# Performance work log

Measured on AMD Instinct MI355X. Metric: run time of the kernel, lower is better.

## Reference

```python
import jax, jax.numpy as jnp
import numpy as np

B, TIN, N, F = 2, 12, 800, 2
H, D = 6, 8
C = H * D          # 48
TP = 10            # prediction steps (= pre_step)
PS5 = TP // 5      # int(pre_step/5) = 2
KW = PS5 + 12      # conv1 kernel width = 14


def setup_inputs() -> dict:
    key = jax.random.key(0)
    it = iter(jax.random.split(key, 40))
    def rn(shape, s=0.1):
        return jax.random.normal(next(it), shape, dtype=jnp.float32) * s
    inp = {}
    inp['x'] = rn((B, TIN, N, F), 1.0)
    inp['T'] = rn((B, TP, N, F - 1), 1.0)
    inp['adj'] = jnp.ones((N, N), dtype=bool)  # softmax(laplace) != 0 is all-True
    for nm in ['Wq_t', 'Wk_t', 'Wv_t', 'Wq_st', 'Wk_st', 'Wv_st']:
        inp[nm] = rn((H, F, D))
    for nm in ['bq_t', 'bk_t', 'bv_t', 'bq_st', 'bk_st', 'bv_st']:
        inp[nm] = rn((H, D))
    inp['conv1_w'] = rn((C, F, 1, KW))
    inp['conv1_b'] = rn((C,))
    inp['Wproj_t'] = rn((C, C)); inp['bproj_t'] = rn((C,))
    inp['Wproj_st'] = rn((C, C)); inp['bproj_st'] = rn((C,))
    for nm in ['xhr_wz', 'xhr_wr', 'xhr_wh']:
        inp[nm] = rn((TIN, 3 * C, C))     # input 2C concat hidden C
    for nm in ['xhr_bz', 'xhr_br', 'xhr_bh']:
        inp[nm] = rn((TIN, N, C))
    for nm in ['last_wz', 'last_wr', 'last_wh']:
        inp[nm] = rn((TP, 2 * C, C))      # input C concat hidden C
    for nm in ['last_bz', 'last_br', 'last_bh']:
        inp[nm] = rn((TP, N, C))
    inp['Wout'] = rn((C, 1)); inp['bout'] = rn((1,))
    return inp


def _gru(xi, h, wz, bz, wr, br, wh, bh):
    xh = jnp.concatenate([xi, h], axis=-1)
    z = jax.nn.sigmoid(xh @ wz + bz)
    r = jax.nn.sigmoid(xh @ wr + br)
    hh = jnp.tanh(jnp.concatenate([xi, r * h], axis=-1) @ wh + bh)
    return (1.0 - z) * h + z * hh


def _forward(adj, x, T, Wq_t, bq_t, Wk_t, bk_t, Wv_t, bv_t,
             Wq_st, bq_st, Wk_st, bk_st, Wv_st, bv_st,
             conv1_w, conv1_b, Wproj_t, bproj_t, Wproj_st, bproj_st,
             xhr_wz, xhr_bz, xhr_wr, xhr_br, xhr_wh, xhr_bh,
             last_wz, last_bz, last_wr, last_br, last_wh, last_bh, Wout, bout):
    scale = 1.0 / np.sqrt(D)
    adjf = adj.astype(jnp.float32)
    # ---- temporal multi-head attention (causal over time, per node) ----
    q = jnp.einsum('btnf,hfd->btnhd', x, Wq_t) + bq_t
    k = jnp.einsum('btnf,hfd->btnhd', x, Wk_t) + bk_t
    v = jnp.einsum('btnf,hfd->btnhd', x, Wv_t) + bv_t
    s = jnp.einsum('btnhd,bsnhd->bnhts', q, k) * scale
    causal = jnp.tril(jnp.ones((TIN, TIN), dtype=bool))
    s = jnp.where(causal, s, -1e9)
    p = jax.nn.softmax(s, axis=-1)
    att_t = jnp.einsum('bnhts,bsnhd->btnhd', p, v).reshape(B, TIN, N, C)
    # ---- spatial multi-head attention (adjacency-weighted, per timestep) ----
    q = jnp.einsum('btnf,hfd->btnhd', x, Wq_st) + bq_st
    k = jnp.einsum('btnf,hfd->btnhd', x, Wk_st) + bk_st
    v = jnp.einsum('btnf,hfd->btnhd', x, Wv_st) + bv_st
    s = jnp.einsum('btnhd,btmhd->bthnm', q, k) * scale
    s = s * adjf  # multiplicative adjacency mask (NOT -inf fill), as in source
    p = jax.nn.softmax(s, axis=-1)
    att_st = jnp.einsum('bthnm,btmhd->btnhd', p, v).reshape(B, TIN, N, C)
    att_stt = jnp.concatenate([att_t @ Wproj_t + bproj_t,
                               att_st @ Wproj_st + bproj_st], axis=-1)  # [B,TIN,N,2C]
    # ---- encoder GRU stack over timesteps 1..TIN-1, cell i has own weights ----
    h0 = jnp.zeros((B, N, C), dtype=x.dtype)
    seq = jnp.swapaxes(att_stt[:, 1:], 0, 1)  # [TIN-1, B, N, 2C]
    def step(h, inp):
        xi, wz, bz, wr, br, wh, bh = inp
        return _gru(xi, h, wz, bz, wr, br, wh, bh), None
    ht, _ = jax.lax.scan(step, h0, (seq, xhr_wz[1:], xhr_bz[1:], xhr_wr[1:],
                                    xhr_br[1:], xhr_wh[1:], xhr_bh[1:]))
    # ---- conv1 over time-extended input ----
    Tcat = jnp.concatenate([jnp.zeros(T.shape[:-1] + (1,), T.dtype), T], axis=-1)
    tpx = jnp.concatenate([x, Tcat], axis=1)                 # [B, TIN+TP, N, F]
    tpx = jnp.concatenate([tpx, tpx[:, :PS5 - 1]], axis=1)   # [B, TIN+TP+PS5-1, N, F]
    lhs = jnp.transpose(tpx, (0, 3, 2, 1))                   # [B, F, N, Ttot]
    conv = jax.lax.conv_general_dilated(lhs, conv1_w, (1, 1), 'VALID',
                                        dimension_numbers=('NCHW', 'OIHW', 'NCHW'))
    pre = jnp.transpose(conv + conv1_b[None, :, None, None], (0, 3, 2, 1))  # [B,TP,N,C]
    # ---- decoder GRU, one cell per step, collecting states ----
    def step2(h, inp):
        xi, wz, bz, wr, br, wh, bh = inp
        h = _gru(xi, h, wz, bz, wr, br, wh, bh)
        return h, h
    _, outs = jax.lax.scan(step2, ht, (jnp.swapaxes(pre, 0, 1), last_wz, last_bz,
                                       last_wr, last_br, last_wh, last_bh))
    out = jnp.swapaxes(outs, 0, 1)  # [B, TP, N, C]
    return out @ Wout + bout        # [B, TP, N, 1]


def reference(x, T, adj, Wq_t, bq_t, Wk_t, bk_t, Wv_t, bv_t,
              Wq_st, bq_st, Wk_st, bk_st, Wv_st, bv_st,
              conv1_w, conv1_b, Wproj_t, bproj_t, Wproj_st, bproj_st,
              xhr_wz, xhr_bz, xhr_wr, xhr_br, xhr_wh, xhr_bh,
              last_wz, last_bz, last_wr, last_br, last_wh, last_bh, Wout, bout):
    return _forward(adj, x, T, Wq_t, bq_t, Wk_t, bk_t, Wv_t, bv_t,
                    Wq_st, bq_st, Wk_st, bk_st, Wv_st, bv_st,
                    conv1_w, conv1_b, Wproj_t, bproj_t, Wproj_st, bproj_st,
                    xhr_wz, xhr_bz, xhr_wr, xhr_br, xhr_wh, xhr_bh,
                    last_wz, last_bz, last_wr, last_br, last_wh, last_bh, Wout, bout)
```

## Files before the change

kernel.cpp:

```cpp
#include <hip/hip_runtime.h>
#include <hip/hip_bf16.h>

typedef __hip_bfloat16 bf16;
typedef __attribute__((ext_vector_type(8))) short s8b;
typedef __attribute__((ext_vector_type(4))) float f4;

#define B_ 2
#define TIN_ 12
#define N_ 800
#define F_ 2
#define H_ 6
#define D_ 8
#define C_ 48
#define TP_ 10
#define KW_ 14
#define SCALE 0.35355339059327373f
#define LOG2E 1.4426950408889634f

__device__ __forceinline__ float sigm(float x) { return 1.0f / (1.0f + __expf(-x)); }
__device__ __forceinline__ float tanh_(float x) {
  float e = __expf(-2.0f * x);
  return 2.0f / (1.0f + e) - 1.0f;
}
__device__ __forceinline__ float exp2_(float x) { return __builtin_amdgcn_exp2f(x); }
__device__ __forceinline__ float bfu(unsigned short u) {
  return __uint_as_float((unsigned)u << 16);
}
__device__ __forceinline__ unsigned short f2u(float v) {
  return __bfloat16_as_ushort(__float2bfloat16(v));
}
__device__ __forceinline__ float ldc(const float* p, size_t i) { return p[i]; }
__device__ __forceinline__ float ldc(const bf16* p, size_t i) { return __bfloat162float(p[i]); }
__device__ __forceinline__ void sto(float* p, size_t i, float v) { p[i] = v; }
__device__ __forceinline__ void sto(bf16* p, size_t i, float v) { p[i] = __float2bfloat16(v); }
__device__ __forceinline__ void gll16(const void* g, void* l) {
  __builtin_amdgcn_global_load_lds(
      (__attribute__((address_space(1))) void*)(g),
      (__attribute__((address_space(3))) void*)(l), 16, 0, 0);
}
__device__ __forceinline__ int detect_f32(const void* xv) {
  const unsigned int* xw = (const unsigned int*)xv;
  unsigned int w = xw[threadIdx.x & 63];
  int e = (w >> 7) & 0xFF;
  int bad = ((e >= 1 && e < 96) || (e > 150)) ? 1 : 0;
  unsigned long long m = __ballot(bad);
  return (__popcll(m) >= 16) ? 1 : 0;
}

template <typename TI>
__device__ __forceinline__ void pack_body(
    int gid, const TI* xwz, const TI* xwr, const TI* xwh,
    const TI* lwz, const TI* lwr, const TI* lwh, bf16* pwb) {
  const int total = 21 * 9216;
  if (gid >= total) return;
  int step = gid / 9216, r = gid % 9216;
  int g = r / 3072;  r %= 3072;
  int nt = r / 1024; r %= 1024;
  int c = r / 512;   r %= 512;
  int lane = r / 8, j = r % 8;
  int k = 32 * c + (lane >> 4) * 8 + j;
  int n = nt * 16 + (lane & 15);
  float v = 0.f;
  if (k < 48) {
    if (step < 11) {
      int t = step + 1;
      const TI* w = (g == 0) ? xwz : (g == 1) ? xwr : xwh;
      v = ldc(w, ((size_t)t * 144 + 96 + k) * 48 + n);
    } else {
      int t = step - 11;
      const TI* w = (g == 0) ? lwz : (g == 1) ? lwr : lwh;
      v = ldc(w, ((size_t)t * 96 + 48 + k) * 48 + n);
    }
  }
  pwb[gid] = __float2bfloat16(v);
}

template <typename TI>
__device__ __forceinline__ void temporal_body(
    int gid, const TI* x, const TI* Wq, const TI* Wk, const TI* Wv,
    const TI* bq, const TI* bk, const TI* bv, bf16* att_t) {
  const int total = B_ * (TIN_ - 1) * H_ * N_;
  if (gid >= total) return;
  int n = gid % N_;
  int r = gid / N_;
  int h = r % H_;  r /= H_;
  int t = (r % (TIN_ - 1)) + 1;
  int b = r / (TIN_ - 1);

  float wq[F_][D_], wk[F_][D_], wv[F_][D_], bqv[D_], bkv[D_], bvv[D_];
#pragma unroll
  for (int f = 0; f < F_; ++f)
#pragma unroll
    for (int d = 0; d < D_; ++d) {
      wq[f][d] = ldc(Wq, (h * F_ + f) * D_ + d);
      wk[f][d] = ldc(Wk, (h * F_ + f) * D_ + d);
      wv[f][d] = ldc(Wv, (h * F_ + f) * D_ + d);
    }
#pragma unroll
  for (int d = 0; d < D_; ++d) {
    bqv[d] = ldc(bq, h * D_ + d);
    bkv[d] = ldc(bk, h * D_ + d);
    bvv[d] = ldc(bv, h * D_ + d);
  }
  float xt0 = ldc(x, ((b * TIN_ + t) * N_ + n) * F_ + 0);
  float xt1 = ldc(x, ((b * TIN_ + t) * N_ + n) * F_ + 1);
  float q[D_];
#pragma unroll
  for (int d = 0; d < D_; ++d) q[d] = xt0 * wq[0][d] + xt1 * wq[1][d] + bqv[d];

  float sc[TIN_];
  float mx = -1e30f;
#pragma unroll
  for (int s = 0; s < TIN_; ++s) {
    float xs0 = ldc(x, ((b * TIN_ + s) * N_ + n) * F_ + 0);
    float xs1 = ldc(x, ((b * TIN_ + s) * N_ + n) * F_ + 1);
    float dot = 0.f;
#pragma unroll
    for (int d = 0; d < D_; ++d)
      dot += q[d] * (xs0 * wk[0][d] + xs1 * wk[1][d] + bkv[d]);
    dot *= SCALE;
    sc[s] = (s <= t) ? dot : -1e30f;
    mx = fmaxf(mx, sc[s]);
  }
  float sum = 0.f;
#pragma unroll
  for (int s = 0; s < TIN_; ++s) {
    float p = __expf(sc[s] - mx);
    sc[s] = p;
    sum += p;
  }
  float inv = 1.0f / sum;
  float acc[D_];
#pragma unroll
  for (int d = 0; d < D_; ++d) acc[d] = 0.f;
#pragma unroll
  for (int s = 0; s < TIN_; ++s) {
    float xs0 = ldc(x, ((b * TIN_ + s) * N_ + n) * F_ + 0);
    float xs1 = ldc(x, ((b * TIN_ + s) * N_ + n) * F_ + 1);
#pragma unroll
    for (int d = 0; d < D_; ++d)
      acc[d] += sc[s] * (xs0 * wv[0][d] + xs1 * wv[1][d] + bvv[d]);
  }
  bf16* o = att_t + ((size_t)((b * 11 + (t - 1)) * N_ + n)) * C_ + h * D_;
#pragma unroll
  for (int d = 0; d < D_; ++d) o[d] = __float2bfloat16(acc[d] * inv);
}

template <typename TI>
__device__ __forceinline__ void spatial4_body(
    float2* xs, float (*M)[9], float (*Vw)[3][D_],
    int tile, int ty, int b, int hg,
    const TI* x, const TI* Wq, const TI* Wk, const TI* Wv,
    const TI* bq, const TI* bk, const TI* bv, bf16* att_st) {
  int t = ty + 1;
  int tid = threadIdx.x;

  for (int m = tid; m < N_; m += 832)
    xs[m] = make_float2(ldc(x, ((b * TIN_ + t) * N_ + m) * F_ + 0),
                        ldc(x, ((b * TIN_ + t) * N_ + m) * F_ + 1));
  if (tid < 18) {
    int lh = tid / 9, e = tid % 9, a = e / 3, bb = e % 3;
    int h = hg * 2 + lh;
    float acc = 0.f;
    for (int d = 0; d < 8; ++d) {
      float qa = (a == 0) ? ldc(Wq, (h * 2 + 0) * 8 + d)
               : (a == 1) ? ldc(Wq, (h * 2 + 1) * 8 + d) : ldc(bq, h * 8 + d);
      float kb = (bb == 0) ? ldc(Wk, (h * 2 + 0) * 8 + d)
               : (bb == 1) ? ldc(Wk, (h * 2 + 1) * 8 + d) : ldc(bk, h * 8 + d);
      acc += qa * kb;
    }
    M[lh][e] = acc * SCALE * LOG2E;
  }
  if (tid >= 64 && tid < 64 + 48) {
    int e = tid - 64;
    int lh = e / 24, a = (e % 24) / 8, d = e % 8;
    int h = hg * 2 + lh;
    Vw[lh][a][d] = (a == 0) ? ldc(Wv, (h * 2 + 0) * 8 + d)
                 : (a == 1) ? ldc(Wv, (h * 2 + 1) * 8 + d) : ldc(bv, h * 8 + d);
  }
  __syncthreads();
  if (tid < 800) {
    int row = tid >> 3, ms = tid & 7;
    int n = tile * 100 + row;
    float x0 = xs[n].x, x1 = xs[n].y;
    float A[2], Bc[2], Cc[2];
#pragma unroll
    for (int lh = 0; lh < 2; ++lh) {
      A[lh]  = M[lh][0] * x0 + M[lh][3] * x1 + M[lh][6];
      Bc[lh] = M[lh][1] * x0 + M[lh][4] * x1 + M[lh][7];
      Cc[lh] = M[lh][2] * x0 + M[lh][5] * x1 + M[lh][8];
    }
    float Sp[2] = {0, 0}, S0[2] = {0, 0}, S1[2] = {0, 0};
    for (int m = ms * 100; m < ms * 100 + 100; ++m) {
      float2 xm = xs[m];
#pragma unroll
      for (int lh = 0; lh < 2; ++lh) {
        float p = exp2_(A[lh] * xm.x + Bc[lh] * xm.y + Cc[lh]);
        Sp[lh] += p;
        S0[lh] += p * xm.x;
        S1[lh] += p * xm.y;
      }
    }
#pragma unroll
    for (int lh = 0; lh < 2; ++lh) {
#pragma unroll
      for (int off = 1; off < 8; off <<= 1) {
        Sp[lh] += __shfl_xor(Sp[lh], off);
        S0[lh] += __shfl_xor(S0[lh], off);
        S1[lh] += __shfl_xor(S1[lh], off);
      }
    }
    if (ms == 0) {
      bf16* o = att_st + ((size_t)((b * 11 + ty) * N_ + n)) * C_;
#pragma unroll
      for (int lh = 0; lh < 2; ++lh) {
        int h = hg * 2 + lh;
        float inv = 1.f / Sp[lh];
#pragma unroll
        for (int d = 0; d < 8; ++d)
          o[h * 8 + d] = __float2bfloat16(
              (S0[lh] * Vw[lh][0][d] + S1[lh] * Vw[lh][1][d] + Sp[lh] * Vw[lh][2][d]) * inv);
      }
    }
  }
}

#define SP_BLKS 528
#define TMP_BLKS 127
#define PK_BLKS 233
__global__ __launch_bounds__(832) void k_phase1(
    const void* x,
    const void* Wq_t, const void* Wk_t, const void* Wv_t,
    const void* bq_t, const void* bk_t, const void* bv_t,
    const void* Wq_st, const void* Wk_st, const void* Wv_st,
    const void* bq_st, const void* bk_st, const void* bv_st,
    const void* xwz, const void* xwr, const void* xwh,
    const void* lwz, const void* lwr, const void* lwh,
    bf16* att_t, bf16* att_st, bf16* pwb) {
  __shared__ float2 xs[N_];
  __shared__ float M[2][9];
  __shared__ float Vw[2][3][D_];
  int f32 = detect_f32(x);
  int bx = blockIdx.x;
  if (bx < SP_BLKS) {
    int tile = bx % 8, ty = (bx / 8) % 11, zz = bx / 88;
    int b = zz / 3, hg = zz % 3;
    if (f32)
      spatial4_body<float>(xs, M, Vw, tile, ty, b, hg,
                           (const float*)x, (const float*)Wq_st, (const float*)Wk_st,
                           (const float*)Wv_st, (const float*)bq_st, (const float*)bk_st,
                           (const float*)bv_st, att_st);
    else
      spatial4_body<bf16>(xs, M, Vw, tile, ty, b, hg,
                          (const bf16*)x, (const bf16*)Wq_st, (const bf16*)Wk_st,
                          (const bf16*)Wv_st, (const bf16*)bq_st, (const bf16*)bk_st,
                          (const bf16*)bv_st, att_st);
  } else if (bx < SP_BLKS + TMP_BLKS) {
    int gid = (bx - SP_BLKS) * 832 + threadIdx.x;
    if (f32)
      temporal_body<float>(gid, (const float*)x, (const float*)Wq_t, (const float*)Wk_t,
                           (const float*)Wv_t, (const float*)bq_t, (const float*)bk_t,
                           (const float*)bv_t, att_t);
    else
      temporal_body<bf16>(gid, (const bf16*)x, (const bf16*)Wq_t, (const bf16*)Wk_t,
                          (const bf16*)Wv_t, (const bf16*)bq_t, (const bf16*)bk_t,
                          (const bf16*)bv_t, att_t);
  } else {
    int gid = (bx - SP_BLKS - TMP_BLKS) * 832 + threadIdx.x;
    if (f32)
      pack_body<float>(gid, (const float*)xwz, (const float*)xwr, (const float*)xwh,
                       (const float*)lwz, (const float*)lwr, (const float*)lwh, pwb);
    else
      pack_body<bf16>(gid, (const bf16*)xwz, (const bf16*)xwr, (const bf16*)xwh,
                      (const bf16*)lwz, (const bf16*)lwr, (const bf16*)lwh, pwb);
  }
}

template <typename TI>
__device__ __forceinline__ void projx2_body(
    unsigned short (*rawT)[72], unsigned short (*rawS)[72], unsigned short (*catS)[104],
    int tile, int ty, int b,
    const bf16* att_t, const bf16* att_st,
    const TI* Wpt, const TI* bpt, const TI* Wps, const TI* bps,
    const TI* xwz, const TI* xwr, const TI* xwh,
    const TI* xbz, const TI* xbr, const TI* xbh,
    bf16* xfrag) {
  int t = ty + 1;
  int tid = threadIdx.x;
  int wv = tid >> 6, l = tid & 63;
  int cg = l >> 4, cl = l & 15;

  for (int e = tid; e < 64 * 72; e += 192) {
    int rr = e / 72, c = e % 72;
    int n = tile * 64 + rr; if (n > 799) n = 799;
    size_t base = ((size_t)((b * 11 + ty) * N_ + n)) * C_;
    rawT[rr][c] = (c < 48) ? __bfloat16_as_ushort(att_t[base + c]) : (unsigned short)0;
    rawS[rr][c] = (c < 48) ? __bfloat16_as_ushort(att_st[base + c]) : (unsigned short)0;
  }
  __syncthreads();
#pragma unroll
  for (int q = 0; q < 2; ++q) {
    int nt = 2 * wv + q;
    int half = nt / 3;
    int ncol = (nt - half * 3) * 16 + cl;
    float bias = half ? ldc(bps, ncol) : ldc(bpt, ncol);
    s8b Bf0, Bf1;
#pragma unroll
    for (int j = 0; j < 8; ++j) {
      int k0 = cg * 8 + j;
      int k1 = 32 + cg * 8 + j;
      Bf0[j] = (short)f2u(half ? ldc(Wps, (size_t)k0 * 48 + ncol)
                               : ldc(Wpt, (size_t)k0 * 48 + ncol));
      Bf1[j] = (k1 < 48) ? (short)f2u(half ? ldc(Wps, (size_t)k1 * 48 + ncol)
                                           : ldc(Wpt, (size_t)k1 * 48 + ncol))
                         : (short)0;
    }
    unsigned short (*raw)[72] = half ? rawS : rawT;
#pragma unroll
    for (int mt = 0; mt < 4; ++mt) {
      s8b A0 = *(const s8b*)&raw[mt * 16 + cl][cg * 8];
      s8b A1 = *(const s8b*)&raw[mt * 16 + cl][32 + cg * 8];
      f4 acc = {bias, bias, bias, bias};
      acc = __builtin_amdgcn_mfma_f32_16x16x32_bf16(A0, Bf0, acc, 0, 0, 0);
      acc = __builtin_amdgcn_mfma_f32_16x16x32_bf16(A1, Bf1, acc, 0, 0, 0);
#pragma unroll
      for (int r = 0; r < 4; ++r)
        catS[mt * 16 + cg * 4 + r][nt * 16 + cl] = f2u(acc[r]);
    }
  }
  __syncthreads();
#pragma unroll
  for (int q = 0; q < 3; ++q) {
    int nt = 3 * wv + q;
    int g = nt / 3;
    int jj = (nt - g * 3) * 16 + cl;
    const TI* wx = (g == 0) ? xwz : (g == 1) ? xwr : xwh;
    const TI* bx = (g == 0) ? xbz : (g == 1) ? xbr : xbh;
    s8b Bf[3];
#pragma unroll
    for (int c = 0; c < 3; ++c)
#pragma unroll
      for (int j = 0; j < 8; ++j) {
        int k = c * 32 + cg * 8 + j;
        Bf[c][j] = (short)f2u(ldc(wx, ((size_t)t * 144 + k) * 48 + jj));
      }
#pragma unroll
    for (int mt = 0; mt < 4; ++mt) {
      int nbase = tile * 64 + mt * 16;
      if (nbase >= 800) continue;
      s8b A0 = *(const s8b*)&catS[mt * 16 + cl][cg * 8];
      s8b A1 = *(const s8b*)&catS[mt * 16 + cl][32 + cg * 8];
      s8b A2 = *(const s8b*)&catS[mt * 16 + cl][64 + cg * 8];
      f4 acc;
#pragma unroll
      for (int r = 0; r < 4; ++r)
        acc[r] = ldc(bx, ((size_t)t * N_ + (nbase + cg * 4 + r)) * C_ + jj);
      acc = __builtin_amdgcn_mfma_f32_16x16x32_bf16(A0, Bf[0], acc, 0, 0, 0);
      acc = __builtin_amdgcn_mfma_f32_16x16x32_bf16(A1, Bf[1], acc, 0, 0, 0);
      acc = __builtin_amdgcn_mfma_f32_16x16x32_bf16(A2, Bf[2], acc, 0, 0, 0);
      int grp = b * 50 + tile * 4 + mt;
      size_t idx = ((((size_t)grp * 21 + ty) * 9 + nt) * 64 + l) * 4;
      ushort4 u;
      u.x = f2u(acc[0]); u.y = f2u(acc[1]); u.z = f2u(acc[2]); u.w = f2u(acc[3]);
      *(ushort4*)((unsigned short*)xfrag + idx) = u;
    }
  }
}

template <typename TI>
__device__ __forceinline__ void convx5_body(
    float (*tpw)[KW_][2], float (*cw)[KW_][48], unsigned short (*preS)[72],
    int tile, int t, int b,
    const TI* x, const TI* T,
    const TI* conv1_w, const TI* conv1_b,
    const TI* lwz, const TI* lwr, const TI* lwh,
    const TI* lbz, const TI* lbr, const TI* lbh,
    bf16* xfrag) {
  int tid = threadIdx.x;
  int wv = tid >> 6, l = tid & 63;
  int cg = l >> 4, cl = l & 15;
  int rw = tid / 12, jl = tid % 12;

#pragma unroll 7
  for (int p = 0; p < 7; ++p) {
    int e = tid + p * 192;
    int f = e / (KW_ * 48), rem = e % (KW_ * 48), k = rem / 48, c = rem % 48;
    cw[f][k][c] = ldc(conv1_w, (c * F_ + f) * KW_ + k);
  }
#pragma unroll 10
  for (int p = 0; p < 10; ++p) {
    int e = tid + p * 192;
    if (e < 64 * KW_ * 2) {
      int rr = e / (KW_ * 2), rem = e % (KW_ * 2), k = rem / 2, f = rem % 2;
      int n = tile * 64 + rr; if (n > 799) n = 799;
      int tau = t + k;
      float v;
      if (tau < TIN_) v = ldc(x, ((size_t)(b * TIN_ + tau) * N_ + n) * F_ + f);
      else if (tau < TIN_ + TP_) v = (f == 0) ? 0.f : ldc(T, (size_t)(b * TP_ + (tau - TIN_)) * N_ + n);
      else v = ldc(x, ((size_t)(b * TIN_ + 0) * N_ + n) * F_ + f);
      tpw[rr][k][f] = v;
    }
  }
  for (int e = tid; e < 64 * 24; e += 192)
    preS[e / 24][48 + e % 24] = 0;
  __syncthreads();
  {
    int c0 = jl * 4;
    float acc[4][4];
#pragma unroll
    for (int qq = 0; qq < 4; ++qq)
#pragma unroll
      for (int m = 0; m < 4; ++m) acc[qq][m] = ldc(conv1_b, c0 + m);
#pragma unroll
    for (int f = 0; f < 2; ++f)
      for (int k = 0; k < KW_; ++k) {
        const float4 w4 = *(const float4*)&cw[f][k][c0];
        float wvv[4] = {w4.x, w4.y, w4.z, w4.w};
#pragma unroll
        for (int qq = 0; qq < 4; ++qq) {
          float tv = tpw[rw * 4 + qq][k][f];
#pragma unroll
          for (int m = 0; m < 4; ++m) acc[qq][m] += tv * wvv[m];
        }
      }
#pragma unroll
    for (int qq = 0; qq < 4; ++qq)
#pragma unroll
      for (int m = 0; m < 4; ++m)
        preS[rw * 4 + qq][c0 + m] = f2u(acc[qq][m]);
  }
  __syncthreads();
#pragma unroll
  for (int q = 0; q < 3; ++q) {
    int nt = 3 * wv + q;
    int g = nt / 3;
    int jj = (nt - g * 3) * 16 + cl;
    const TI* wl = (g == 0) ? lwz : (g == 1) ? lwr : lwh;
    const TI* bl = (g == 0) ? lbz : (g == 1) ? lbr : lbh;
    s8b Bf0, Bf1;
#pragma unroll
    for (int j = 0; j < 8; ++j) {
      int k0 = cg * 8 + j;
      int k1 = 32 + cg * 8 + j;
      Bf0[j] = (short)f2u(ldc(wl, ((size_t)t * 96 + k0) * 48 + jj));
      Bf1[j] = (k1 < 48) ? (short)f2u(ldc(wl, ((size_t)t * 96 + k1) * 48 + jj)) : (short)0;
    }
#pragma unroll
    for (int mt = 0; mt < 4; ++mt) {
      int nbase = tile * 64 + mt * 16;
      if (nbase >= 800) continue;
      s8b A0 = *(const s8b*)&preS[mt * 16 + cl][cg * 8];
      s8b A1 = *(const s8b*)&preS[mt * 16 + cl][32 + cg * 8];
      f4 acc;
#pragma unroll
      for (int r = 0; r < 4; ++r)
        acc[r] = ldc(bl, ((size_t)t * N_ + (nbase + cg * 4 + r)) * C_ + jj);
      acc = __builtin_amdgcn_mfma_f32_16x16x32_bf16(A0, Bf0, acc, 0, 0, 0);
      acc = __builtin_amdgcn_mfma_f32_16x16x32_bf16(A1, Bf1, acc, 0, 0, 0);
      int grp = b * 50 + tile * 4 + mt;
      size_t idx = ((((size_t)grp * 21 + (11 + t)) * 9 + nt) * 64 + l) * 4;
      ushort4 u;
      u.x = f2u(acc[0]); u.y = f2u(acc[1]); u.z = f2u(acc[2]); u.w = f2u(acc[3]);
      *(ushort4*)((unsigned short*)xfrag + idx) = u;
    }
  }
}

#define PJ_BLKS 286
#define CV_BLKS 260
__global__ __launch_bounds__(192) void k_xc(
    const bf16* att_t, const bf16* att_st,
    const void* Wpt, const void* bpt, const void* Wps, const void* bps,
    const void* xwz, const void* xwr, const void* xwh,
    const void* xbz, const void* xbr, const void* xbh,
    const void* x, const void* T, const void* cw_, const void* cb,
    const void* lwz, const void* lwr, const void* lwh,
    const void* lbz, const void* lbr, const void* lbh, bf16* xfrag) {
  __shared__ __align__(16) char smem[31744];
  int f32 = detect_f32(x);
  int bx = blockIdx.x;
  if (bx < PJ_BLKS) {
    int tile = bx % 13, ty = (bx / 13) % 11, b = bx / 143;
    auto rawT = (unsigned short(*)[72])smem;
    auto rawS = (unsigned short(*)[72])(smem + 9216);
    auto catS = (unsigned short(*)[104])(smem + 18432);
    if (f32)
      projx2_body<float>(rawT, rawS, catS, tile, ty, b, att_t, att_st,
                         (const float*)Wpt, (const float*)bpt, (const float*)Wps,
                         (const float*)bps, (const float*)xwz, (const float*)xwr,
                         (const float*)xwh, (const float*)xbz, (const float*)xbr,
                         (const float*)xbh, xfrag);
    else
      projx2_body<bf16>(rawT, rawS, catS, tile, ty, b, att_t, att_st,
                        (const bf16*)Wpt, (const bf16*)bpt, (const bf16*)Wps,
                        (const bf16*)bps, (const bf16*)xwz, (const bf16*)xwr,
                        (const bf16*)xwh, (const bf16*)xbz, (const bf16*)xbr,
                        (const bf16*)xbh, xfrag);
  } else {
    int cblk = bx - PJ_BLKS;
    int tile = cblk % 13, t = (cblk / 13) % 10, b = cblk / 130;
    auto tpw  = (float(*)[KW_][2])smem;
    auto cw   = (float(*)[KW_][48])(smem + 7168);
    auto preS = (unsigned short(*)[72])(smem + 12544);
    if (f32)
      convx5_body<float>(tpw, cw, preS, tile, t, b,
                         (const float*)x, (const float*)T, (const float*)cw_, (const float*)cb,
                         (const float*)lwz, (const float*)lwr, (const float*)lwh,
                         (const float*)lbz, (const float*)lbr, (const float*)lbh, xfrag);
    else
      convx5_body<bf16>(tpw, cw, preS, tile, t, b,
                        (const bf16*)x, (const bf16*)T, (const bf16*)cw_, (const bf16*)cb,
                        (const bf16*)lwz, (const bf16*)lwr, (const bf16*)lwh,
                        (const bf16*)lbz, (const bf16*)lbr, (const bf16*)lbh, xfrag);
  }
}

template <typename TI, typename TO>
__device__ __forceinline__ void gru11_body(
    unsigned short (*wbuf)[9216], unsigned short (*xbuf)[2560],
    unsigned short* hT, unsigned short* rhT,
    const unsigned short* xfrag, const unsigned short* pwb,
    const TI* Wout, const TI* bout, TO* out) {
  int l = threadIdx.x;
  int cg = l >> 4, cl = l & 15;
  int blk = blockIdx.x;
  int b = blk / 50;
  int n0 = (blk % 50) * 16;

  for (int e = l; e < 1152; e += 64) { hT[e] = 0; rhT[e] = 0; }
  float bo = ldc(bout, 0);
  s8b WoB0, WoB1;
#pragma unroll
  for (int j = 0; j < 8; ++j) {
    int k0 = cg * 8 + j;
    int k1 = 32 + cg * 8 + j;
    WoB0[j] = (cl == 0) ? (short)f2u(ldc(Wout, k0)) : (short)0;
    WoB1[j] = (cl == 0 && k1 < 48) ? (short)f2u(ldc(Wout, k1)) : (short)0;
  }
  float ho[3][4];
#pragma unroll
  for (int nt = 0; nt < 3; ++nt)
#pragma unroll
    for (int r = 0; r < 4; ++r) ho[nt][r] = 0.f;

  const unsigned short* xg = xfrag + (size_t)blk * 48384;
#pragma unroll
  for (int i = 0; i < 18; ++i) gll16(pwb + i * 512 + l * 8, &wbuf[0][i * 512]);
#pragma unroll
  for (int i = 0; i < 5; ++i) gll16(xg + i * 512 + l * 8, &xbuf[0][i * 512]);
  asm volatile("" ::: "memory");

  for (int step = 0; step < 21; ++step) {
    int cur = step & 1;
    s8b hA0 = *(const s8b*)&hT[cl * 72 + cg * 8];
    s8b hA1 = *(const s8b*)&hT[cl * 72 + 32 + cg * 8];
    if (step >= 12) {
      f4 oacc = {bo, bo, bo, bo};
      oacc = __builtin_amdgcn_mfma_f32_16x16x32_bf16(hA0, WoB0, oacc, 0, 0, 0);
      oacc = __builtin_amdgcn_mfma_f32_16x16x32_bf16(hA1, WoB1, oacc, 0, 0, 0);
      if (cl == 0) {
        int t = step - 12;
#pragma unroll
        for (int r = 0; r < 4; ++r)
          sto(out, ((size_t)b * TP_ + t) * N_ + n0 + cg * 4 + r, oacc[r]);
      }
    }
    asm volatile("s_waitcnt vmcnt(0)" ::: "memory");
    s8b Wz[3][2], Wr[3][2], Wh[3][2];
    const unsigned short* wb = wbuf[cur];
#pragma unroll
    for (int nt = 0; nt < 3; ++nt)
#pragma unroll
      for (int c = 0; c < 2; ++c) {
        Wz[nt][c] = *(const s8b*)&wb[0 * 3072 + nt * 1024 + c * 512 + l * 8];
        Wr[nt][c] = *(const s8b*)&wb[1 * 3072 + nt * 1024 + c * 512 + l * 8];
        Wh[nt][c] = *(const s8b*)&wb[2 * 3072 + nt * 1024 + c * 512 + l * 8];
      }
    ushort4 cx[9];
#pragma unroll
    for (int gn = 0; gn < 9; ++gn)
      cx[gn] = *(const ushort4*)&xbuf[cur][gn * 256 + l * 4];
    if (step < 20) {
      const unsigned short* wsn = pwb + (size_t)(step + 1) * 9216;
#pragma unroll
      for (int i = 0; i < 18; ++i) gll16(wsn + i * 512 + l * 8, &wbuf[cur ^ 1][i * 512]);
      const unsigned short* xsn = xg + (size_t)(step + 1) * 2304;
#pragma unroll
      for (int i = 0; i < 5; ++i) gll16(xsn + i * 512 + l * 8, &xbuf[cur ^ 1][i * 512]);
    }
    f4 az[3], ar[3];
#pragma unroll
    for (int nt = 0; nt < 3; ++nt) {
      f4 cz = {bfu(cx[nt].x), bfu(cx[nt].y), bfu(cx[nt].z), bfu(cx[nt].w)};
      cz = __builtin_amdgcn_mfma_f32_16x16x32_bf16(hA0, Wz[nt][0], cz, 0, 0, 0);
      cz = __builtin_amdgcn_mfma_f32_16x16x32_bf16(hA1, Wz[nt][1], cz, 0, 0, 0);
      az[nt] = cz;
      f4 cr = {bfu(cx[3 + nt].x), bfu(cx[3 + nt].y), bfu(cx[3 + nt].z), bfu(cx[3 + nt].w)};
      cr = __builtin_amdgcn_mfma_f32_16x16x32_bf16(hA0, Wr[nt][0], cr, 0, 0, 0);
      cr = __builtin_amdgcn_mfma_f32_16x16x32_bf16(hA1, Wr[nt][1], cr, 0, 0, 0);
      ar[nt] = cr;
    }
    float z[3][4];
#pragma unroll
    for (int nt = 0; nt < 3; ++nt)
#pragma unroll
      for (int r = 0; r < 4; ++r) {
        z[nt][r] = sigm(az[nt][r]);
        float rv = sigm(ar[nt][r]) * ho[nt][r];
        rhT[(cg * 4 + r) * 72 + nt * 16 + cl] = f2u(rv);
      }
    asm volatile("" ::: "memory");
    s8b rA0 = *(const s8b*)&rhT[cl * 72 + cg * 8];
    s8b rA1 = *(const s8b*)&rhT[cl * 72 + 32 + cg * 8];
    f4 ah[3];
#pragma unroll
    for (int nt = 0; nt < 3; ++nt) {
      f4 ch = {bfu(cx[6 + nt].x), bfu(cx[6 + nt].y), bfu(cx[6 + nt].z), bfu(cx[6 + nt].w)};
      ch = __builtin_amdgcn_mfma_f32_16x16x32_bf16(rA0, Wh[nt][0], ch, 0, 0, 0);
      ch = __builtin_amdgcn_mfma_f32_16x16x32_bf16(rA1, Wh[nt][1], ch, 0, 0, 0);
      ah[nt] = ch;
    }
#pragma unroll
    for (int nt = 0; nt < 3; ++nt)
#pragma unroll
      for (int r = 0; r < 4; ++r) {
        float hn = (1.f - z[nt][r]) * ho[nt][r] + z[nt][r] * tanh_(ah[nt][r]);
        ho[nt][r] = hn;
        hT[(cg * 4 + r) * 72 + nt * 16 + cl] = f2u(hn);
      }
    asm volatile("" ::: "memory");
  }
  {
    s8b hA0 = *(const s8b*)&hT[cl * 72 + cg * 8];
    s8b hA1 = *(const s8b*)&hT[cl * 72 + 32 + cg * 8];
    f4 oacc = {bo, bo, bo, bo};
    oacc = __builtin_amdgcn_mfma_f32_16x16x32_bf16(hA0, WoB0, oacc, 0, 0, 0);
    oacc = __builtin_amdgcn_mfma_f32_16x16x32_bf16(hA1, WoB1, oacc, 0, 0, 0);
    if (cl == 0) {
#pragma unroll
      for (int r = 0; r < 4; ++r)
        sto(out, ((size_t)b * TP_ + 9) * N_ + n0 + cg * 4 + r, oacc[r]);
    }
  }
}
__global__ __launch_bounds__(64) void k_gru11(
    const void* xin, const bf16* xfrag, const bf16* pwb,
    const void* Wout, const void* bout, void* out) {
  __shared__ alignas(16) unsigned short wbuf[2][9216];
  __shared__ alignas(16) unsigned short xbuf[2][2560];
  __shared__ alignas(16) unsigned short hT[1152];
  __shared__ alignas(16) unsigned short rhT[1152];
  int f32 = detect_f32(xin);
  if (f32)
    gru11_body<float, float>(wbuf, xbuf, hT, rhT,
                             (const unsigned short*)xfrag, (const unsigned short*)pwb,
                             (const float*)Wout, (const float*)bout, (float*)out);
  else
    gru11_body<bf16, bf16>(wbuf, xbuf, hT, rhT,
                           (const unsigned short*)xfrag, (const unsigned short*)pwb,
                           (const bf16*)Wout, (const bf16*)bout, (bf16*)out);
}

extern "C" void kernel_launch(void* const* d_in, const int* in_sizes, int n_in,
                              void* d_out, int out_size, void* d_ws, size_t ws_size,
                              hipStream_t stream) {
  (void)in_sizes; (void)n_in; (void)out_size; (void)ws_size;
  const void* x       = d_in[0];
  const void* T       = d_in[1];
  const void* Wq_t    = d_in[3];
  const void* Wk_t    = d_in[4];
  const void* Wv_t    = d_in[5];
  const void* Wq_st   = d_in[6];
  const void* Wk_st   = d_in[7];
  const void* Wv_st   = d_in[8];
  const void* bq_t    = d_in[9];
  const void* bk_t    = d_in[10];
  const void* bv_t    = d_in[11];
  const void* bq_st   = d_in[12];
  const void* bk_st   = d_in[13];
  const void* bv_st   = d_in[14];
  const void* conv1_w = d_in[15];
  const void* conv1_b = d_in[16];
  const void* Wproj_t = d_in[17];
  const void* bproj_t = d_in[18];
  const void* Wproj_st= d_in[19];
  const void* bproj_st= d_in[20];
  const void* xhr_wz  = d_in[21];
  const void* xhr_wr  = d_in[22];
  const void* xhr_wh  = d_in[23];
  const void* xhr_bz  = d_in[24];
  const void* xhr_br  = d_in[25];
  const void* xhr_bh  = d_in[26];
  const void* last_wz = d_in[27];
  const void* last_wr = d_in[28];
  const void* last_wh = d_in[29];
  const void* last_bz = d_in[30];
  const void* last_br = d_in[31];
  const void* last_bh = d_in[32];
  const void* Wout    = d_in[33];
  const void* bout    = d_in[34];

  char* wsb = (char*)d_ws;
  bf16* att_t  = (bf16*)(wsb + 256);
  bf16* att_st = att_t + (size_t)2 * 11 * 800 * 48;
  bf16* xfrag  = att_st + (size_t)2 * 11 * 800 * 48;
  bf16* pwb    = xfrag + (size_t)100 * 21 * 9 * 64 * 4;

  k_phase1<<<SP_BLKS + TMP_BLKS + PK_BLKS, 832, 0, stream>>>(
      x, Wq_t, Wk_t, Wv_t, bq_t, bk_t, bv_t,
      Wq_st, Wk_st, Wv_st, bq_st, bk_st, bv_st,
      xhr_wz, xhr_wr, xhr_wh, last_wz, last_wr, last_wh,
      att_t, att_st, pwb);
  k_xc<<<PJ_BLKS + CV_BLKS, 192, 0, stream>>>(
      att_t, att_st, Wproj_t, bproj_t, Wproj_st, bproj_st,
      xhr_wz, xhr_wr, xhr_wh, xhr_bz, xhr_br, xhr_bh,
      x, T, conv1_w, conv1_b, last_wz, last_wr, last_wh,
      last_bz, last_br, last_bh, xfrag);
  k_gru11<<<100, 64, 0, stream>>>(
      x, xfrag, pwb, Wout, bout, d_out);
}
```

Before: 119.9 us.

## Prefetch GRU weights and inputs into registers instead of LDS double buffer

The recurrent GRU kernel no longer uses global_load_lds double buffering with explicit vmcnt waits. It loads the next step's weight fragments and input fragments straight into a second register set, then swaps the A/B sets across an unrolled pair of steps. Empty asm pins keep the loads from being sunk, so their latency hides behind the current step's MFMA and activation work. This removes the LDS round trip and the full memory wait at the top of each step, at the cost of many more VGPRs.

```diff
diff --git a/kernel.cpp b/kernel.cpp
--- a/kernel.cpp
+++ b/kernel.cpp
@@ -17,6 +17,8 @@
 #define SCALE 0.35355339059327373f
 #define LOG2E 1.4426950408889634f
 
+#define PIN(v) asm volatile("" :: "v"(v))
+
 __device__ __forceinline__ float sigm(float x) { return 1.0f / (1.0f + __expf(-x)); }
 __device__ __forceinline__ float tanh_(float x) {
   float e = __expf(-2.0f * x);
@@ -33,11 +35,6 @@
 __device__ __forceinline__ float ldc(const bf16* p, size_t i) { return __bfloat162float(p[i]); }
 __device__ __forceinline__ void sto(float* p, size_t i, float v) { p[i] = v; }
 __device__ __forceinline__ void sto(bf16* p, size_t i, float v) { p[i] = __float2bfloat16(v); }
-__device__ __forceinline__ void gll16(const void* g, void* l) {
-  __builtin_amdgcn_global_load_lds(
-      (__attribute__((address_space(1))) void*)(g),
-      (__attribute__((address_space(3))) void*)(l), 16, 0, 0);
-}
 __device__ __forceinline__ int detect_f32(const void* xv) {
   const unsigned int* xw = (const unsigned int*)xv;
   unsigned int w = xw[threadIdx.x & 63];
@@ -515,9 +512,97 @@
   }
 }
 
+template <bool PF, typename TO>
+__device__ __forceinline__ void gru_step12(
+    int step, int l, int cg, int cl, int b, int n0,
+    s8b (&Wzc)[3][2], s8b (&Wrc)[3][2], s8b (&Whc)[3][2], ushort4 (&cxc)[9],
+    s8b (&Wzn)[3][2], s8b (&Wrn)[3][2], s8b (&Whn)[3][2], ushort4 (&cxn)[9],
+    const unsigned short* pwb, const unsigned short* xg,
+    unsigned short* hT, unsigned short* rhT,
+    float (&ho)[3][4], const s8b& WoB0, const s8b& WoB1, float bo, TO* out) {
+  s8b hA0 = *(const s8b*)&hT[cl * 72 + cg * 8];
+  s8b hA1 = *(const s8b*)&hT[cl * 72 + 32 + cg * 8];
+  if (step >= 12) {
+    f4 oacc = {bo, bo, bo, bo};
+    oacc = __builtin_amdgcn_mfma_f32_16x16x32_bf16(hA0, WoB0, oacc, 0, 0, 0);
+    oacc = __builtin_amdgcn_mfma_f32_16x16x32_bf16(hA1, WoB1, oacc, 0, 0, 0);
+    if (cl == 0) {
+      int t = step - 12;
+#pragma unroll
+      for (int r = 0; r < 4; ++r)
+        sto(out, ((size_t)b * TP_ + t) * N_ + n0 + cg * 4 + r, oacc[r]);
+    }
+  }
+  if (PF) {
+    const unsigned short* pb = pwb + (size_t)(step + 1) * 9216 + (size_t)l * 8;
+#pragma unroll
+    for (int nt = 0; nt < 3; ++nt)
+#pragma unroll
+      for (int c = 0; c < 2; ++c) {
+        Wzn[nt][c] = *(const s8b*)(pb + 0 * 3072 + nt * 1024 + c * 512);
+        Wrn[nt][c] = *(const s8b*)(pb + 1 * 3072 + nt * 1024 + c * 512);
+        Whn[nt][c] = *(const s8b*)(pb + 2 * 3072 + nt * 1024 + c * 512);
+      }
+    const unsigned short* xsrc = xg + (size_t)(step + 1) * 2304 + (size_t)l * 4;
+#pragma unroll
+    for (int gn = 0; gn < 9; ++gn)
+      cxn[gn] = *(const ushort4*)(xsrc + gn * 256);
+  }
+  f4 az[3], ar[3];
+#pragma unroll
+  for (int nt = 0; nt < 3; ++nt) {
+    f4 cz = {bfu(cxc[nt].x), bfu(cxc[nt].y), bfu(cxc[nt].z), bfu(cxc[nt].w)};
+    cz = __builtin_amdgcn_mfma_f32_16x16x32_bf16(hA0, Wzc[nt][0], cz, 0, 0, 0);
+    cz = __builtin_amdgcn_mfma_f32_16x16x32_bf16(hA1, Wzc[nt][1], cz, 0, 0, 0);
+    az[nt] = cz;
+    f4 cr = {bfu(cxc[3 + nt].x), bfu(cxc[3 + nt].y), bfu(cxc[3 + nt].z), bfu(cxc[3 + nt].w)};
+    cr = __builtin_amdgcn_mfma_f32_16x16x32_bf16(hA0, Wrc[nt][0], cr, 0, 0, 0);
+    cr = __builtin_amdgcn_mfma_f32_16x16x32_bf16(hA1, Wrc[nt][1], cr, 0, 0, 0);
+    ar[nt] = cr;
+  }
+  float z[3][4];
+#pragma unroll
+  for (int nt = 0; nt < 3; ++nt)
+#pragma unroll
+    for (int r = 0; r < 4; ++r) {
+      z[nt][r] = sigm(az[nt][r]);
+      float rv = sigm(ar[nt][r]) * ho[nt][r];
+      rhT[(cg * 4 + r) * 72 + nt * 16 + cl] = f2u(rv);
+    }
+  asm volatile("" ::: "memory");
+  s8b rA0 = *(const s8b*)&rhT[cl * 72 + cg * 8];
+  s8b rA1 = *(const s8b*)&rhT[cl * 72 + 32 + cg * 8];
+  f4 ah[3];
+#pragma unroll
+  for (int nt = 0; nt < 3; ++nt) {
+    f4 ch = {bfu(cxc[6 + nt].x), bfu(cxc[6 + nt].y), bfu(cxc[6 + nt].z), bfu(cxc[6 + nt].w)};
+    ch = __builtin_amdgcn_mfma_f32_16x16x32_bf16(rA0, Whc[nt][0], ch, 0, 0, 0);
+    ch = __builtin_amdgcn_mfma_f32_16x16x32_bf16(rA1, Whc[nt][1], ch, 0, 0, 0);
+    ah[nt] = ch;
+  }
+#pragma unroll
+  for (int nt = 0; nt < 3; ++nt)
+#pragma unroll
+    for (int r = 0; r < 4; ++r) {
+      float hn = (1.f - z[nt][r]) * ho[nt][r] + z[nt][r] * tanh_(ah[nt][r]);
+      ho[nt][r] = hn;
+      hT[(cg * 4 + r) * 72 + nt * 16 + cl] = f2u(hn);
+    }
+  asm volatile("" ::: "memory");
+  if (PF) {
+#pragma unroll
+    for (int nt = 0; nt < 3; ++nt)
+#pragma unroll
+      for (int c = 0; c < 2; ++c) {
+        PIN(Wzn[nt][c]); PIN(Wrn[nt][c]); PIN(Whn[nt][c]);
+      }
+#pragma unroll
+    for (int gn = 0; gn < 9; ++gn) PIN(cxn[gn]);
+  }
+}
+
 template <typename TI, typename TO>
-__device__ __forceinline__ void gru11_body(
-    unsigned short (*wbuf)[9216], unsigned short (*xbuf)[2560],
+__device__ __forceinline__ void gru12_body(
     unsigned short* hT, unsigned short* rhT,
     const unsigned short* xfrag, const unsigned short* pwb,
     const TI* Wout, const TI* bout, TO* out) {
@@ -544,92 +629,37 @@
     for (int r = 0; r < 4; ++r) ho[nt][r] = 0.f;
 
   const unsigned short* xg = xfrag + (size_t)blk * 48384;
-#pragma unroll
-  for (int i = 0; i < 18; ++i) gll16(pwb + i * 512 + l * 8, &wbuf[0][i * 512]);
-#pragma unroll
-  for (int i = 0; i < 5; ++i) gll16(xg + i * 512 + l * 8, &xbuf[0][i * 512]);
+  s8b WzA[3][2], WrA[3][2], WhA[3][2];
+  s8b WzB[3][2], WrB[3][2], WhB[3][2];
+  ushort4 cxA[9], cxB[9];
+  {
+    const unsigned short* pb = pwb + (size_t)l * 8;
+#pragma unroll
+    for (int nt = 0; nt < 3; ++nt)
+#pragma unroll
+      for (int c = 0; c < 2; ++c) {
+        WzA[nt][c] = *(const s8b*)(pb + 0 * 3072 + nt * 1024 + c * 512);
+        WrA[nt][c] = *(const s8b*)(pb + 1 * 3072 + nt * 1024 + c * 512);
+        WhA[nt][c] = *(const s8b*)(pb + 2 * 3072 + nt * 1024 + c * 512);
+      }
+#pragma unroll
+    for (int gn = 0; gn < 9; ++gn)
+      cxA[gn] = *(const ushort4*)(xg + gn * 256 + l * 4);
+  }
   asm volatile("" ::: "memory");
 
-  for (int step = 0; step < 21; ++step) {
-    int cur = step & 1;
-    s8b hA0 = *(const s8b*)&hT[cl * 72 + cg * 8];
-    s8b hA1 = *(const s8b*)&hT[cl * 72 + 32 + cg * 8];
-    if (step >= 12) {
-      f4 oacc = {bo, bo, bo, bo};
-      oacc = __builtin_amdgcn_mfma_f32_16x16x32_bf16(hA0, WoB0, oacc, 0, 0, 0);
-      oacc = __builtin_amdgcn_mfma_f32_16x16x32_bf16(hA1, WoB1, oacc, 0, 0, 0);
-      if (cl == 0) {
-        int t = step - 12;
-#pragma unroll
-        for (int r = 0; r < 4; ++r)
-          sto(out, ((size_t)b * TP_ + t) * N_ + n0 + cg * 4 + r, oacc[r]);
-      }
-    }
-    asm volatile("s_waitcnt vmcnt(0)" ::: "memory");
-    s8b Wz[3][2], Wr[3][2], Wh[3][2];
-    const unsigned short* wb = wbuf[cur];
-#pragma unroll
-    for (int nt = 0; nt < 3; ++nt)
-#pragma unroll
-      for (int c = 0; c < 2; ++c) {
-        Wz[nt][c] = *(const s8b*)&wb[0 * 3072 + nt * 1024 + c * 512 + l * 8];
-        Wr[nt][c] = *(const s8b*)&wb[1 * 3072 + nt * 1024 + c * 512 + l * 8];
-        Wh[nt][c] = *(const s8b*)&wb[2 * 3072 + nt * 1024 + c * 512 + l * 8];
-      }
-    ushort4 cx[9];
-#pragma unroll
-    for (int gn = 0; gn < 9; ++gn)
-      cx[gn] = *(const ushort4*)&xbuf[cur][gn * 256 + l * 4];
-    if (step < 20) {
-      const unsigned short* wsn = pwb + (size_t)(step + 1) * 9216;
-#pragma unroll
-      for (int i = 0; i < 18; ++i) gll16(wsn + i * 512 + l * 8, &wbuf[cur ^ 1][i * 512]);
-      const unsigned short* xsn = xg + (size_t)(step + 1) * 2304;
-#pragma unroll
-      for (int i = 0; i < 5; ++i) gll16(xsn + i * 512 + l * 8, &xbuf[cur ^ 1][i * 512]);
-    }
-    f4 az[3], ar[3];
-#pragma unroll
-    for (int nt = 0; nt < 3; ++nt) {
-      f4 cz = {bfu(cx[nt].x), bfu(cx[nt].y), bfu(cx[nt].z), bfu(cx[nt].w)};
-      cz = __builtin_amdgcn_mfma_f32_16x16x32_bf16(hA0, Wz[nt][0], cz, 0, 0, 0);
-      cz = __builtin_amdgcn_mfma_f32_16x16x32_bf16(hA1, Wz[nt][1], cz, 0, 0, 0);
-      az[nt] = cz;
-      f4 cr = {bfu(cx[3 + nt].x), bfu(cx[3 + nt].y), bfu(cx[3 + nt].z), bfu(cx[3 + nt].w)};
-      cr = __builtin_amdgcn_mfma_f32_16x16x32_bf16(hA0, Wr[nt][0], cr, 0, 0, 0);
-      cr = __builtin_amdgcn_mfma_f32_16x16x32_bf16(hA1, Wr[nt][1], cr, 0, 0, 0);
-      ar[nt] = cr;
-    }
-    float z[3][4];
-#pragma unroll
-    for (int nt = 0; nt < 3; ++nt)
-#pragma unroll
-      for (int r = 0; r < 4; ++r) {
-        z[nt][r] = sigm(az[nt][r]);
-        float rv = sigm(ar[nt][r]) * ho[nt][r];
-        rhT[(cg * 4 + r) * 72 + nt * 16 + cl] = f2u(rv);
-      }
-    asm volatile("" ::: "memory");
-    s8b rA0 = *(const s8b*)&rhT[cl * 72 + cg * 8];
-    s8b rA1 = *(const s8b*)&rhT[cl * 72 + 32 + cg * 8];
-    f4 ah[3];
-#pragma unroll
-    for (int nt = 0; nt < 3; ++nt) {
-      f4 ch = {bfu(cx[6 + nt].x), bfu(cx[6 + nt].y), bfu(cx[6 + nt].z), bfu(cx[6 + nt].w)};
-      ch = __builtin_amdgcn_mfma_f32_16x16x32_bf16(rA0, Wh[nt][0], ch, 0, 0, 0);
-      ch = __builtin_amdgcn_mfma_f32_16x16x32_bf16(rA1, Wh[nt][1], ch, 0, 0, 0);
-      ah[nt] = ch;
-    }
-#pragma unroll
-    for (int nt = 0; nt < 3; ++nt)
-#pragma unroll
-      for (int r = 0; r < 4; ++r) {
-        float hn = (1.f - z[nt][r]) * ho[nt][r] + z[nt][r] * tanh_(ah[nt][r]);
-        ho[nt][r] = hn;
-        hT[(cg * 4 + r) * 72 + nt * 16 + cl] = f2u(hn);
-      }
-    asm volatile("" ::: "memory");
-  }
+#pragma unroll 1
+  for (int s2 = 0; s2 < 10; ++s2) {
+    gru_step12<true>(2 * s2, l, cg, cl, b, n0,
+                     WzA, WrA, WhA, cxA, WzB, WrB, WhB, cxB,
+                     pwb, xg, hT, rhT, ho, WoB0, WoB1, bo, out);
+    gru_step12<true>(2 * s2 + 1, l, cg, cl, b, n0,
+                     WzB, WrB, WhB, cxB, WzA, WrA, WhA, cxA,
+                     pwb, xg, hT, rhT, ho, WoB0, WoB1, bo, out);
+  }
+  gru_step12<false>(20, l, cg, cl, b, n0,
+                    WzA, WrA, WhA, cxA, WzB, WrB, WhB, cxB,
+                    pwb, xg, hT, rhT, ho, WoB0, WoB1, bo, out);
   {
     s8b hA0 = *(const s8b*)&hT[cl * 72 + cg * 8];
     s8b hA1 = *(const s8b*)&hT[cl * 72 + 32 + cg * 8];
@@ -643,20 +673,18 @@
     }
   }
 }
-__global__ __launch_bounds__(64) void k_gru11(
+__global__ __launch_bounds__(64, 1) void k_gru12(
     const void* xin, const bf16* xfrag, const bf16* pwb,
     const void* Wout, const void* bout, void* out) {
-  __shared__ alignas(16) unsigned short wbuf[2][9216];
-  __shared__ alignas(16) unsigned short xbuf[2][2560];
   __shared__ alignas(16) unsigned short hT[1152];
   __shared__ alignas(16) unsigned short rhT[1152];
   int f32 = detect_f32(xin);
   if (f32)
-    gru11_body<float, float>(wbuf, xbuf, hT, rhT,
+    gru12_body<float, float>(hT, rhT,
                              (const unsigned short*)xfrag, (const unsigned short*)pwb,
                              (const float*)Wout, (const float*)bout, (float*)out);
   else
-    gru11_body<bf16, bf16>(wbuf, xbuf, hT, rhT,
+    gru12_body<bf16, bf16>(hT, rhT,
                            (const unsigned short*)xfrag, (const unsigned short*)pwb,
                            (const bf16*)Wout, (const bf16*)bout, (bf16*)out);
 }
@@ -716,6 +744,6 @@
       xhr_wz, xhr_wr, xhr_wh, xhr_bz, xhr_br, xhr_bh,
       x, T, conv1_w, conv1_b, last_wz, last_wr, last_wh,
       last_bz, last_br, last_bh, xfrag);
-  k_gru11<<<100, 64, 0, stream>>>(
+  k_gru12<<<100, 64, 0, stream>>>(
       x, xfrag, pwb, Wout, bout, d_out);
 }
```

Result: no change. 117.7 us (-1.9%).
